# Kernel tuning notes

Measured on AMD Instinct MI355X. Metric: run time of the kernel, lower is better.

## Reference

```python
import jax, jax.numpy as jnp
import numpy as np

B, N, M = 1024, 1024, 64


def setup_inputs() -> dict:
    key = jax.random.key(0)
    ks = jax.random.split(key, 9)
    return {
        "memory": jax.random.normal(ks[0], (B, N, M), dtype=jnp.float32),
        "k": jax.random.normal(ks[1], (B, M), dtype=jnp.float32),
        "beta": jax.random.uniform(ks[2], (B, 1), dtype=jnp.float32),
        "g": jax.random.uniform(ks[3], (B, 1), dtype=jnp.float32),
        "s": jax.random.uniform(ks[4], (B, 3), dtype=jnp.float32),
        "gamma": jax.random.uniform(ks[5], (B, 1), dtype=jnp.float32),
        "w_prev": jax.random.uniform(ks[6], (B, N), dtype=jnp.float32),
        "e": jax.random.uniform(ks[7], (B, M), dtype=jnp.float32),
        "a": jax.random.normal(ks[8], (B, M), dtype=jnp.float32),
    }


def reference(memory, k, beta, g, s, gamma, w_prev, e, a):
    EPS = 1e-16
    COS_EPS = 1e-8  # torch cosine_similarity norm clamp

    # --- _similarity: content addressing (cosine sim + softmax over N) ---
    mem_e = memory + EPS                      # (B, N, M)
    k_e = (k + EPS)[:, None, :]               # (B, 1, M)
    dot = jnp.sum(mem_e * k_e, axis=-1)       # (B, N)
    denom = (jnp.maximum(jnp.linalg.norm(mem_e, axis=-1), COS_EPS)
             * jnp.maximum(jnp.linalg.norm(k_e, axis=-1), COS_EPS))
    wc = jax.nn.softmax(beta * (dot / denom), axis=1)  # (B, N)

    # --- _interpolate ---
    wg = g * wc + (1.0 - g) * w_prev           # (B, N)

    # --- _shift: 3-tap circular convolution, vectorized over batch ---
    # c[i] = s[0]*w[i-1] + s[1]*w[i] + s[2]*w[i+1]  (circular)
    w_hat = (s[:, 0:1] * jnp.roll(wg, 1, axis=1)
             + s[:, 1:2] * wg
             + s[:, 2:3] * jnp.roll(wg, -1, axis=1))

    # --- _sharpen ---
    w = w_hat ** gamma
    w = w / (jnp.sum(w, axis=1, keepdims=True) + EPS)  # (B, N)

    # --- read ---
    read = jnp.einsum('bn,bnm->bm', w, memory)         # (B, M)

    # --- write: rank-1 erase / add ---
    erase = w[:, :, None] * e[:, None, :]              # (B, N, M)
    add = w[:, :, None] * a[:, None, :]                # (B, N, M)
    new_mem = memory * (1.0 - erase) + add             # (B, N, M)

    # pack read (as an extra row) with the updated memory: (B, N+1, M)
    return jnp.concatenate([read[:, None, :], new_mem], axis=1)
```

## Files before the change

### kernel.cpp

```cpp
#include <hip/hip_runtime.h>
#include <cmath>

#define NB 1024
#define NN 1024
#define MM 64
#define NT 256

__device__ __forceinline__ float block_sum(float v, float* s_tmp) {
    #pragma unroll
    for (int off = 32; off > 0; off >>= 1) v += __shfl_xor(v, off, 64);
    if ((threadIdx.x & 63) == 0) s_tmp[threadIdx.x >> 6] = v;
    __syncthreads();
    float r = s_tmp[0] + s_tmp[1] + s_tmp[2] + s_tmp[3];
    __syncthreads();
    return r;
}

__device__ __forceinline__ float block_max(float v, float* s_tmp) {
    #pragma unroll
    for (int off = 32; off > 0; off >>= 1) v = fmaxf(v, __shfl_xor(v, off, 64));
    if ((threadIdx.x & 63) == 0) s_tmp[threadIdx.x >> 6] = v;
    __syncthreads();
    float r = fmaxf(fmaxf(s_tmp[0], s_tmp[1]), fmaxf(s_tmp[2], s_tmp[3]));
    __syncthreads();
    return r;
}

__global__ void __launch_bounds__(NT) ntm_fused(
    const float* __restrict__ memory,
    const float* __restrict__ k,
    const float* __restrict__ beta,
    const float* __restrict__ g,
    const float* __restrict__ s,
    const float* __restrict__ gamma,
    const float* __restrict__ w_prev,
    const float* __restrict__ e,
    const float* __restrict__ a,
    float* __restrict__ out)
{
    __shared__ float  s_wg[NN];
    __shared__ float  s_w[NN];
    __shared__ float  s_k[MM];
    __shared__ float  s_tmp[4];
    __shared__ float4 s_red[NT];

    const int b  = blockIdx.x;
    const int t  = threadIdx.x;
    const int cg = t & 15;
    const int rg = t >> 4;

    const float* memb = memory + (size_t)b * NN * MM;
    float*       outb = out    + (size_t)b * (NN + 1) * MM;

    if (t < MM) s_k[t] = k[b * MM + t] + 1e-16f;
    __syncthreads();
    float kq = (t < MM) ? s_k[t] * s_k[t] : 0.0f;
    float kden = fmaxf(sqrtf(block_sum(kq, s_tmp)), 1e-8f);
    const float bet = beta[b];
    const float4 k4 = ((const float4*)s_k)[cg];

    for (int it = 0; it < NN / 16; ++it) {
        int n = it * 16 + rg;
        float4 m4 = *(const float4*)(memb + n * MM + 4 * cg);
        float ex = m4.x + 1e-16f, ey = m4.y + 1e-16f;
        float ez = m4.z + 1e-16f, ew = m4.w + 1e-16f;
        float d = ex * k4.x + ey * k4.y + ez * k4.z + ew * k4.w;
        float q = ex * ex + ey * ey + ez * ez + ew * ew;
        #pragma unroll
        for (int off = 8; off > 0; off >>= 1) {
            d += __shfl_xor(d, off, 64);
            q += __shfl_xor(q, off, 64);
        }
        if (cg == 0) {
            float denom = fmaxf(sqrtf(q), 1e-8f) * kden;
            s_wg[n] = bet * d / denom;
        }
    }
    __syncthreads();

    float sc0 = s_wg[t], sc1 = s_wg[t + 256], sc2 = s_wg[t + 512], sc3 = s_wg[t + 768];
    float mx = block_max(fmaxf(fmaxf(sc0, sc1), fmaxf(sc2, sc3)), s_tmp);
    float e0 = __expf(sc0 - mx), e1 = __expf(sc1 - mx);
    float e2 = __expf(sc2 - mx), e3 = __expf(sc3 - mx);
    float inv_esum = 1.0f / block_sum(e0 + e1 + e2 + e3, s_tmp);

    const float gb = g[b], omg = 1.0f - gb;
    s_wg[t]       = gb * e0 * inv_esum + omg * w_prev[b * NN + t];
    s_wg[t + 256] = gb * e1 * inv_esum + omg * w_prev[b * NN + t + 256];
    s_wg[t + 512] = gb * e2 * inv_esum + omg * w_prev[b * NN + t + 512];
    s_wg[t + 768] = gb * e3 * inv_esum + omg * w_prev[b * NN + t + 768];
    __syncthreads();

    const float s0 = s[b * 3 + 0], s1 = s[b * 3 + 1], s2 = s[b * 3 + 2];
    const float gam = gamma[b];
    float wpart = 0.0f;
    #pragma unroll
    for (int j = 0; j < 4; ++j) {
        int n  = t + j * 256;
        int nm = (n == 0) ? NN - 1 : n - 1;
        int np = (n == NN - 1) ? 0 : n + 1;
        float wh = s0 * s_wg[nm] + s1 * s_wg[n] + s2 * s_wg[np];
        float w  = powf(wh, gam);
        s_w[n] = w;
        wpart += w;
    }
    float winv = 1.0f / (block_sum(wpart, s_tmp) + 1e-16f);
    #pragma unroll
    for (int j = 0; j < 4; ++j) s_w[t + j * 256] *= winv;
    __syncthreads();

    const float4 e4 = *(const float4*)(e + b * MM + 4 * cg);
    const float4 a4 = *(const float4*)(a + b * MM + 4 * cg);
    float4 acc = make_float4(0.f, 0.f, 0.f, 0.f);
    for (int it = 0; it < NN / 16; ++it) {
        int n = it * 16 + rg;
        float4 m4 = *(const float4*)(memb + n * MM + 4 * cg);
        float wn = s_w[n];
        acc.x += wn * m4.x; acc.y += wn * m4.y;
        acc.z += wn * m4.z; acc.w += wn * m4.w;
        float4 o;
        o.x = m4.x * (1.0f - wn * e4.x) + wn * a4.x;
        o.y = m4.y * (1.0f - wn * e4.y) + wn * a4.y;
        o.z = m4.z * (1.0f - wn * e4.z) + wn * a4.z;
        o.w = m4.w * (1.0f - wn * e4.w) + wn * a4.w;
        *(float4*)(outb + (n + 1) * MM + 4 * cg) = o;
    }

    s_red[t] = acc;
    __syncthreads();
    if (t < 16) {
        float4 r = make_float4(0.f, 0.f, 0.f, 0.f);
        #pragma unroll
        for (int gi = 0; gi < 16; ++gi) {
            float4 v = s_red[gi * 16 + t];
            r.x += v.x; r.y += v.y; r.z += v.z; r.w += v.w;
        }
        *(float4*)(outb + 4 * t) = r;
    }
}

extern "C" void kernel_launch(void* const* d_in, const int* in_sizes, int n_in,
                              void* d_out, int out_size, void* d_ws, size_t ws_size,
                              hipStream_t stream) {
    ntm_fused<<<NB, NT, 0, stream>>>(
        (const float*)d_in[0],
        (const float*)d_in[1],
        (const float*)d_in[2],
        (const float*)d_in[3],
        (const float*)d_in[4],
        (const float*)d_in[5],
        (const float*)d_in[6],
        (const float*)d_in[7],
        (const float*)d_in[8],
        (float*)d_out);
}
```

Before: 503.0 us.

## Split fused NTM kernel into three kernels with row-sliced blocks for parallelism

Replaces the single per-batch fused kernel with three launches: a scores kernel and an update kernel that each split every batch's 1024 rows across 8 blocks, plus a per-batch weights kernel for softmax, interpolation, shift and sharpen. Intermediate weights go through workspace, or through the output buffer when the workspace is too small. The read vector is accumulated with atomicAdd after being zeroed. This raises block count and short per-block loops to improve latency hiding, at the cost of extra launches, global round-trips for the weights, and atomics.

```diff
diff --git a/kernel.cpp b/kernel.cpp
--- a/kernel.cpp
+++ b/kernel.cpp
@@ -5,6 +5,8 @@
 #define NN 1024
 #define MM 64
 #define NT 256
+#define NSL 8
+#define RPS (NN / NSL)
 
 __device__ __forceinline__ float block_sum(float v, float* s_tmp) {
     #pragma unroll
@@ -26,41 +28,33 @@
     return r;
 }
 
-__global__ void __launch_bounds__(NT) ntm_fused(
+__global__ void __launch_bounds__(NT) k_scores(
     const float* __restrict__ memory,
     const float* __restrict__ k,
     const float* __restrict__ beta,
-    const float* __restrict__ g,
-    const float* __restrict__ s,
-    const float* __restrict__ gamma,
-    const float* __restrict__ w_prev,
-    const float* __restrict__ e,
-    const float* __restrict__ a,
-    float* __restrict__ out)
+    float* __restrict__ wbuf, long bs, long rs)
 {
-    __shared__ float  s_wg[NN];
-    __shared__ float  s_w[NN];
-    __shared__ float  s_k[MM];
-    __shared__ float  s_tmp[4];
-    __shared__ float4 s_red[NT];
-
-    const int b  = blockIdx.x;
+    __shared__ float s_k[MM];
+    __shared__ float s_tmp[4];
+
+    const int b  = blockIdx.x >> 3;
+    const int sl = blockIdx.x & 7;
     const int t  = threadIdx.x;
     const int cg = t & 15;
     const int rg = t >> 4;
 
+    if (t < MM) s_k[t] = k[b * MM + t] + 1e-16f;
+    __syncthreads();
+    float kq = (t < MM) ? s_k[t] * s_k[t] : 0.0f;
+    const float kden = fmaxf(sqrtf(block_sum(kq, s_tmp)), 1e-8f);
+    const float bet  = beta[b];
+    const float4 k4  = ((const float4*)s_k)[cg];
+
     const float* memb = memory + (size_t)b * NN * MM;
-    float*       outb = out    + (size_t)b * (NN + 1) * MM;
-
-    if (t < MM) s_k[t] = k[b * MM + t] + 1e-16f;
-    __syncthreads();
-    float kq = (t < MM) ? s_k[t] * s_k[t] : 0.0f;
-    float kden = fmaxf(sqrtf(block_sum(kq, s_tmp)), 1e-8f);
-    const float bet = beta[b];
-    const float4 k4 = ((const float4*)s_k)[cg];
-
-    for (int it = 0; it < NN / 16; ++it) {
-        int n = it * 16 + rg;
+    const int n0 = sl * RPS;
+    #pragma unroll
+    for (int it = 0; it < RPS / 16; ++it) {
+        int n = n0 + it * 16 + rg;
         float4 m4 = *(const float4*)(memb + n * MM + 4 * cg);
         float ex = m4.x + 1e-16f, ey = m4.y + 1e-16f;
         float ez = m4.z + 1e-16f, ew = m4.w + 1e-16f;
@@ -73,12 +67,31 @@
         }
         if (cg == 0) {
             float denom = fmaxf(sqrtf(q), 1e-8f) * kden;
-            s_wg[n] = bet * d / denom;
+            wbuf[(size_t)b * bs + (size_t)n * rs] = bet * d / denom;
         }
     }
-    __syncthreads();
-
-    float sc0 = s_wg[t], sc1 = s_wg[t + 256], sc2 = s_wg[t + 512], sc3 = s_wg[t + 768];
+}
+
+__global__ void __launch_bounds__(NT) k_weights(
+    const float* __restrict__ g,
+    const float* __restrict__ s,
+    const float* __restrict__ gamma,
+    const float* __restrict__ w_prev,
+    float* __restrict__ wbuf, long bs, long rs,
+    float* __restrict__ out)
+{
+    __shared__ float s_wg[NN];
+    __shared__ float s_w[NN];
+    __shared__ float s_tmp[4];
+
+    const int b = blockIdx.x;
+    const int t = threadIdx.x;
+    float* wb = wbuf + (size_t)b * bs;
+
+    float sc0 = wb[(size_t)(t      ) * rs];
+    float sc1 = wb[(size_t)(t + 256) * rs];
+    float sc2 = wb[(size_t)(t + 512) * rs];
+    float sc3 = wb[(size_t)(t + 768) * rs];
     float mx = block_max(fmaxf(fmaxf(sc0, sc1), fmaxf(sc2, sc3)), s_tmp);
     float e0 = __expf(sc0 - mx), e1 = __expf(sc1 - mx);
     float e2 = __expf(sc2 - mx), e3 = __expf(sc3 - mx);
@@ -106,16 +119,45 @@
     }
     float winv = 1.0f / (block_sum(wpart, s_tmp) + 1e-16f);
     #pragma unroll
-    for (int j = 0; j < 4; ++j) s_w[t + j * 256] *= winv;
-    __syncthreads();
-
+    for (int j = 0; j < 4; ++j) {
+        int n = t + j * 256;
+        wb[(size_t)n * rs] = s_w[n] * winv;
+    }
+    if (t < MM) out[(size_t)b * (NN + 1) * MM + t] = 0.0f;
+}
+
+__global__ void __launch_bounds__(NT) k_update(
+    const float* __restrict__ memory,
+    const float* __restrict__ e,
+    const float* __restrict__ a,
+    const float* __restrict__ wbuf, long bs, long rs,
+    float* __restrict__ out)
+{
+    __shared__ float  s_w[RPS];
+    __shared__ float4 s_red[NT];
+
+    const int b  = blockIdx.x >> 3;
+    const int sl = blockIdx.x & 7;
+    const int t  = threadIdx.x;
+    const int cg = t & 15;
+    const int rg = t >> 4;
+    const int n0 = sl * RPS;
+
+    if (t < RPS) s_w[t] = wbuf[(size_t)b * bs + (size_t)(n0 + t) * rs];
+    __syncthreads();
+
+    const float* memb = memory + (size_t)b * NN * MM;
+    float*       outb = out    + (size_t)b * (NN + 1) * MM;
     const float4 e4 = *(const float4*)(e + b * MM + 4 * cg);
     const float4 a4 = *(const float4*)(a + b * MM + 4 * cg);
+
     float4 acc = make_float4(0.f, 0.f, 0.f, 0.f);
-    for (int it = 0; it < NN / 16; ++it) {
-        int n = it * 16 + rg;
+    #pragma unroll
+    for (int it = 0; it < RPS / 16; ++it) {
+        int nl = it * 16 + rg;
+        int n  = n0 + nl;
         float4 m4 = *(const float4*)(memb + n * MM + 4 * cg);
-        float wn = s_w[n];
+        float wn = s_w[nl];
         acc.x += wn * m4.x; acc.y += wn * m4.y;
         acc.z += wn * m4.z; acc.w += wn * m4.w;
         float4 o;
@@ -123,7 +165,7 @@
         o.y = m4.y * (1.0f - wn * e4.y) + wn * a4.y;
         o.z = m4.z * (1.0f - wn * e4.z) + wn * a4.z;
         o.w = m4.w * (1.0f - wn * e4.w) + wn * a4.w;
-        *(float4*)(outb + (n + 1) * MM + 4 * cg) = o;
+        *(float4*)(outb + (size_t)(n + 1) * MM + 4 * cg) = o;
     }
 
     s_red[t] = acc;
@@ -135,22 +177,36 @@
             float4 v = s_red[gi * 16 + t];
             r.x += v.x; r.y += v.y; r.z += v.z; r.w += v.w;
         }
-        *(float4*)(outb + 4 * t) = r;
+        atomicAdd(outb + 4 * t + 0, r.x);
+        atomicAdd(outb + 4 * t + 1, r.y);
+        atomicAdd(outb + 4 * t + 2, r.z);
+        atomicAdd(outb + 4 * t + 3, r.w);
     }
 }
 
 extern "C" void kernel_launch(void* const* d_in, const int* in_sizes, int n_in,
                               void* d_out, int out_size, void* d_ws, size_t ws_size,
                               hipStream_t stream) {
-    ntm_fused<<<NB, NT, 0, stream>>>(
-        (const float*)d_in[0],
-        (const float*)d_in[1],
-        (const float*)d_in[2],
-        (const float*)d_in[3],
-        (const float*)d_in[4],
-        (const float*)d_in[5],
-        (const float*)d_in[6],
-        (const float*)d_in[7],
-        (const float*)d_in[8],
-        (float*)d_out);
-}
+    const float* memory = (const float*)d_in[0];
+    const float* k      = (const float*)d_in[1];
+    const float* beta   = (const float*)d_in[2];
+    const float* g      = (const float*)d_in[3];
+    const float* s      = (const float*)d_in[4];
+    const float* gamma  = (const float*)d_in[5];
+    const float* w_prev = (const float*)d_in[6];
+    const float* e      = (const float*)d_in[7];
+    const float* a      = (const float*)d_in[8];
+    float* out = (float*)d_out;
+
+    const size_t need = (size_t)NB * NN * sizeof(float);
+    float* wbuf; long bs, rs;
+    if (ws_size >= need) {
+        wbuf = (float*)d_ws; bs = NN; rs = 1;
+    } else {
+        wbuf = out + MM; bs = (long)(NN + 1) * MM; rs = MM;
+    }
+
+    k_scores <<<NB * NSL, NT, 0, stream>>>(memory, k, beta, wbuf, bs, rs);
+    k_weights<<<NB,       NT, 0, stream>>>(g, s, gamma, w_prev, wbuf, bs, rs, out);
+    k_update <<<NB * NSL, NT, 0, stream>>>(memory, e, a, wbuf, bs, rs, out);
+}
```

Measured after the change: 511.4 us. No clear change (+1.7%).
